# Kernel optimization log

Measured on AMD Instinct MI355X. Metric: run time of the kernel, lower is better.

Reference implementation:

```python
import jax, jax.numpy as jnp
import numpy as np

L, D_MODEL, D_INNER, D_STATE, D_CONV, DT_RANK, NUM_ORDERS = 16384, 192, 384, 16, 4, 12, 2
NUM_BLOCKS = 2 * NUM_ORDERS
EPS = 1e-5


def rmsnorm(x, w):
    return x * jax.lax.rsqrt(jnp.mean(x * x, axis=-1, keepdims=True) + EPS) * w


def layernorm(x, w, b):
    m = jnp.mean(x, axis=-1, keepdims=True)
    v = jnp.mean((x - m) ** 2, axis=-1, keepdims=True)
    return (x - m) * jax.lax.rsqrt(v + EPS) * w + b


def causal_dw_conv(x, w, b):
    # x: [L, d], w: [d, K] causal depthwise conv (small fixed K loop)
    K = w.shape[1]
    xp = jnp.pad(x, ((K - 1, 0), (0, 0)))
    y = b
    for k in range(K):
        y = y + xp[k:k + x.shape[0]] * w[:, k]
    return y


def selective_scan(u, dt, A, B, C, Dskip):
    # u, dt: [L, d]; A: [d, n]; B, C: [L, n]; Dskip: [d]
    def step(h, inp):
        u_t, dt_t, B_t, C_t = inp
        dA = jnp.exp(dt_t[:, None] * A)                    # [d, n]
        h = dA * h + (dt_t * u_t)[:, None] * B_t[None, :]  # [d, n]
        return h, h @ C_t                                  # y_t: [d]
    h0 = jnp.zeros(A.shape, u.dtype)
    _, ys = jax.lax.scan(step, h0, (u, dt, B, C))
    return ys + u * Dskip


def mamba_block(x, nw, Wi, cw, cb, Wx, Wdt, bdt, A_log, Dp, Wo):
    # pre-RMSNorm residual Mamba block (create_block semantics)
    res = x
    h = rmsnorm(x, nw)
    xz = h @ Wi                              # [L, 2*d_inner]
    xc, z = jnp.split(xz, 2, axis=-1)
    xc = jax.nn.silu(causal_dw_conv(xc, cw, cb))
    proj = xc @ Wx                           # [L, dt_rank + 2*d_state]
    dt_raw = proj[:, :DT_RANK]
    B = proj[:, DT_RANK:DT_RANK + D_STATE]
    C = proj[:, DT_RANK + D_STATE:]
    dt = jax.nn.softplus(dt_raw @ Wdt + bdt)
    y = selective_scan(xc, dt, -jnp.exp(A_log), B, C, Dp)
    y = y * jax.nn.silu(z)
    return res + y @ Wo


def setup_inputs() -> dict:
    key = jax.random.key(0)
    ks = jax.random.split(key, 10)
    s = 0.02
    x = jax.random.normal(ks[0], (L, D_MODEL), jnp.float32)
    orders = jnp.stack([
        jax.random.permutation(jax.random.fold_in(ks[1], o), L)
        for o in range(NUM_ORDERS)
    ]).astype(jnp.int32)                                     # [NUM_ORDERS, L]
    norm_w = jnp.ones((NUM_BLOCKS, D_MODEL), jnp.float32)
    in_proj_w = jax.random.normal(ks[2], (NUM_BLOCKS, D_MODEL, 2 * D_INNER), jnp.float32) * s
    conv_w = jax.random.normal(ks[3], (NUM_BLOCKS, D_INNER, D_CONV), jnp.float32) * s
    conv_b = jnp.zeros((NUM_BLOCKS, D_INNER), jnp.float32)
    x_proj_w = jax.random.normal(ks[4], (NUM_BLOCKS, D_INNER, DT_RANK + 2 * D_STATE), jnp.float32) * s
    dt_w = jax.random.normal(ks[5], (NUM_BLOCKS, DT_RANK, D_INNER), jnp.float32) * s
    dt_b = jnp.full((NUM_BLOCKS, D_INNER), np.log(np.expm1(0.01)), jnp.float32)  # softplus^-1(0.01)
    A_log = jnp.log(jnp.broadcast_to(jnp.arange(1, D_STATE + 1, dtype=jnp.float32),
                                     (NUM_BLOCKS, D_INNER, D_STATE)))
    D_p = jnp.ones((NUM_BLOCKS, D_INNER), jnp.float32)
    out_proj_w = jax.random.normal(ks[6], (NUM_BLOCKS, D_INNER, D_MODEL), jnp.float32) * s
    fwd_ln_w = jnp.ones((NUM_ORDERS, D_MODEL), jnp.float32)
    fwd_ln_b = jnp.zeros((NUM_ORDERS, D_MODEL), jnp.float32)
    bwd_ln_w = jnp.ones((NUM_ORDERS, D_MODEL), jnp.float32)
    bwd_ln_b = jnp.zeros((NUM_ORDERS, D_MODEL), jnp.float32)
    out_ln_w = jnp.ones((NUM_ORDERS, D_MODEL), jnp.float32)
    out_ln_b = jnp.zeros((NUM_ORDERS, D_MODEL), jnp.float32)
    return {"x": x, "orders": orders, "norm_w": norm_w, "in_proj_w": in_proj_w,
            "conv_w": conv_w, "conv_b": conv_b, "x_proj_w": x_proj_w,
            "dt_w": dt_w, "dt_b": dt_b, "A_log": A_log, "D_p": D_p,
            "out_proj_w": out_proj_w, "fwd_ln_w": fwd_ln_w, "fwd_ln_b": fwd_ln_b,
            "bwd_ln_w": bwd_ln_w, "bwd_ln_b": bwd_ln_b,
            "out_ln_w": out_ln_w, "out_ln_b": out_ln_b}


def reference(x, orders, norm_w, in_proj_w, conv_w, conv_b, x_proj_w, dt_w, dt_b,
              A_log, D_p, out_proj_w, fwd_ln_w, fwd_ln_b, bwd_ln_w, bwd_ln_b,
              out_ln_w, out_ln_b):
    out = x
    for o in range(NUM_ORDERS):          # small fixed loop over serialization orders
        idx = orders[o]
        xo = x[idx]                      # serialize voxel tokens in this order
        fb, bb = o, NUM_ORDERS + o       # forward / backward block indices
        f = mamba_block(xo, norm_w[fb], in_proj_w[fb], conv_w[fb], conv_b[fb],
                        x_proj_w[fb], dt_w[fb], dt_b[fb], A_log[fb], D_p[fb], out_proj_w[fb])
        b = mamba_block(xo[::-1], norm_w[bb], in_proj_w[bb], conv_w[bb], conv_b[bb],
                        x_proj_w[bb], dt_w[bb], dt_b[bb], A_log[bb], D_p[bb], out_proj_w[bb])[::-1]
        comb = layernorm(f, fwd_ln_w[o], fwd_ln_b[o]) + layernorm(b, bwd_ln_w[o], bwd_ln_b[o])
        comb = layernorm(comb, out_ln_w[o], out_ln_b[o])
        out = out + jnp.zeros_like(x).at[idx].set(comb)  # de-serialize (scatter back)
    return out
```

## Files before the change

kernel.cpp:

```cpp
#include <hip/hip_runtime.h>
#include <math.h>

#define LSEQ 16384
#define DM 192
#define DI 384
#define DSN 16
#define DCONV 4
#define DTRK 12
#define NPROJ 44
#define EPSV 1e-5f
#define TCH 32
#define NCH (LSEQ / TCH)
#define GDIM (DI * DSN)
#define RGRP 8
#define NGRP (NCH / RGRP)
#define CT 8

typedef __attribute__((ext_vector_type(8))) short bf16x8;
typedef __attribute__((ext_vector_type(4))) float f32x4;

__device__ __forceinline__ float siluf(float x) { return x / (1.f + __expf(-x)); }
__device__ __forceinline__ float softplus_f(float x) {
  float e = __expf(x);
  float l = __logf(1.f + e);
  return (x > 20.f) ? x : l;
}
__device__ __forceinline__ ushort f2b(float f) {
  uint u = __float_as_uint(f);
  u += 0x7fff + ((u >> 16) & 1);
  return (ushort)(u >> 16);
}
__device__ __forceinline__ float b2f(ushort h) { return __uint_as_float(((uint)h) << 16); }
__device__ __forceinline__ ushort f2h(float f) { _Float16 h = (_Float16)f; return *(ushort*)&h; }
__device__ __forceinline__ float h2f(ushort u) { _Float16 h = *(_Float16*)&u; return (float)h; }

__device__ __forceinline__ void pow16(float q, float (&a)[16]) {
  float q2 = q*q, q4 = q2*q2, q8 = q4*q4;
  a[0]=q;        a[1]=q2;       a[2]=q2*q;      a[3]=q4;
  a[4]=q4*q;     a[5]=q4*q2;    a[6]=q4*q2*q;   a[7]=q8;
  a[8]=q8*q;     a[9]=q8*q2;    a[10]=q8*q2*q;  a[11]=q8*q4;
  a[12]=q8*q4*q; a[13]=q8*q4*q2;a[14]=q8*q4*q2*q;a[15]=q8*q8;
}

#define PREP_A (4 * 768 * DM)
#define PREP_B (4 * 64 * DI)
#define PREP_C (4 * DM * DI)
__global__ void k_prep(const float* __restrict__ Wi, const float* __restrict__ nw,
                       const float* __restrict__ Wx, const float* __restrict__ Wo,
                       ushort* __restrict__ Wct, ushort* __restrict__ Wxt,
                       ushort* __restrict__ Wot) {
  int i = blockIdx.x * 256 + threadIdx.x;
  if (i < PREP_A) {
    int blk = i / (768 * DM), j = i % (768 * DM);
    int n = j / DM, k = j % DM;
    Wct[i] = f2b(nw[blk*DM + k] * Wi[(size_t)blk*DM*768 + (size_t)k*768 + n]);
  } else if (i < PREP_A + PREP_B) {
    int q = i - PREP_A;
    int blk = q / (64 * DI), j = q % (64 * DI);
    int n = j / DI, k = j % DI;
    Wxt[q] = (n < NPROJ) ? f2b(Wx[(size_t)blk*DI*NPROJ + (size_t)k*NPROJ + n]) : (ushort)0;
  } else if (i < PREP_A + PREP_B + PREP_C) {
    int q = i - PREP_A - PREP_B;
    int blk = q / (DM * DI), j = q % (DM * DI);
    int n = j / DI, k = j % DI;
    Wot[q] = f2b(Wo[(size_t)blk*DI*DM + (size_t)k*DM + n]);
  }
}

__global__ __launch_bounds__(64) void k_gather_rms(const float* __restrict__ x,
                                                   const int* __restrict__ orders,
                                                   ushort* __restrict__ xon) {
  int t = blockIdx.x;
  int o = blockIdx.y;
  int lane = threadIdx.x;
  int r = orders[(size_t)o*LSEQ + t];
  ushort* xo = xon + (size_t)o*LSEQ*DM;
  float v0 = x[(size_t)r*DM + lane];
  float v1 = x[(size_t)r*DM + 64 + lane];
  float v2 = x[(size_t)r*DM + 128 + lane];
  float ss = v0*v0 + v1*v1 + v2*v2;
  #pragma unroll
  for (int oo = 32; oo > 0; oo >>= 1) ss += __shfl_xor(ss, oo);
  float s = rsqrtf(ss * (1.f/DM) + EPSV);
  xo[(size_t)t*DM + lane]       = f2b(v0 * s);
  xo[(size_t)t*DM + 64 + lane]  = f2b(v1 * s);
  xo[(size_t)t*DM + 128 + lane] = f2b(v2 * s);
}

template<int MI, int AMODE, int OMODE>
__global__ __launch_bounds__(256) void k_mm(
    const ushort* __restrict__ A, const ushort* __restrict__ Yp,
    const ushort* __restrict__ Zp, const ushort* __restrict__ Bt,
    void* __restrict__ C0, void* __restrict__ C1,
    int N, int K, int lda, int ldz, int ldc,
    long sA, long sY, long sZ, long sB, long sC)
{
  __shared__ __align__(16) ushort As[32 * MI * 64];
  __shared__ __align__(16) ushort Bs[64 * 64];
  const int z = blockIdx.z;
  if (AMODE == 0) A += (size_t)z * sA;
  else { Yp += (size_t)z * sY; Zp += (size_t)z * sZ; }
  Bt += (size_t)z * sB;
  const int bm = blockIdx.x * (32 * MI), bn = blockIdx.y * 64;
  const int tid = threadIdx.x;
  const int l = tid & 63, w = tid >> 6;
  const int wm = w & 1, wn = w >> 1;
  f32x4 acc[MI][2] = {};

  for (int k0 = 0; k0 < K; k0 += 64) {
    #pragma unroll
    for (int p = 0; p < MI; p++) {
      int c = tid + p * 256;
      int row = c >> 3, ko = (c & 7) * 8;
      int sw = (row * 128 + (c & 7) * 16) ^ ((row & 7) << 4);
      if (AMODE == 0) {
        uint4 v = *(const uint4*)(A + (size_t)(bm + row) * lda + k0 + ko);
        *(uint4*)((char*)As + sw) = v;
      } else {
        const ushort* yrow = Yp + (size_t)(bm + row) * lda + k0 + ko;
        const ushort* zrow = Zp + (size_t)(bm + row) * ldz + k0 + ko;
        ushort tmp[8];
        #pragma unroll
        for (int j = 0; j < 8; j++) {
          float zz = b2f(zrow[j]);
          tmp[j] = f2b(b2f(yrow[j]) * (zz / (1.f + __expf(-zz))));
        }
        *(uint4*)((char*)As + sw) = *(const uint4*)tmp;
      }
    }
    #pragma unroll
    for (int p = 0; p < 2; p++) {
      int c = tid + p * 256;
      int row = c >> 3, ko = (c & 7) * 8;
      int sw = (row * 128 + (c & 7) * 16) ^ ((row & 7) << 4);
      uint4 v = *(const uint4*)(Bt + (size_t)(bn + row) * K + k0 + ko);
      *(uint4*)((char*)Bs + sw) = v;
    }
    __syncthreads();
    #pragma unroll
    for (int ks = 0; ks < 2; ks++) {
      bf16x8 af[MI], bfv[2];
      #pragma unroll
      for (int mi = 0; mi < MI; mi++) {
        int r = 16 * MI * wm + 16 * mi + (l & 15);
        int ad = (r * 128 + 32 * ks + 16 * (l >> 4)) ^ ((r & 7) << 4);
        af[mi] = *(const bf16x8*)((const char*)As + ad);
      }
      #pragma unroll
      for (int ni = 0; ni < 2; ni++) {
        int r = 32 * wn + 16 * ni + (l & 15);
        int ad = (r * 128 + 32 * ks + 16 * (l >> 4)) ^ ((r & 7) << 4);
        bfv[ni] = *(const bf16x8*)((const char*)Bs + ad);
      }
      #pragma unroll
      for (int mi = 0; mi < MI; mi++)
        #pragma unroll
        for (int ni = 0; ni < 2; ni++)
          acc[mi][ni] = __builtin_amdgcn_mfma_f32_16x16x32_bf16(
              af[mi], bfv[ni], acc[mi][ni], 0, 0, 0);
    }
    __syncthreads();
  }

  #pragma unroll
  for (int mi = 0; mi < MI; mi++) {
    #pragma unroll
    for (int ni = 0; ni < 2; ni++) {
      int c0 = bn + 32 * wn + 16 * ni + (l & 15);
      if (OMODE != 2 && c0 >= N) continue;
      int r0 = bm + 16 * MI * wm + 16 * mi + 4 * (l >> 4);
      #pragma unroll
      for (int j = 0; j < 4; j++) {
        if (OMODE == 0) {
          ((float*)C0 + (size_t)z*sC)[(size_t)(r0 + j) * ldc + c0] = acc[mi][ni][j];
        } else if (OMODE == 1) {
          ((ushort*)C0 + (size_t)z*sC)[(size_t)(r0 + j) * ldc + c0] = f2b(acc[mi][ni][j]);
        } else {
          if (c0 < 384)
            ((ushort*)C0 + (size_t)z*sC)[(size_t)(r0 + j) * 384 + c0] = f2b(acc[mi][ni][j]);
          else
            ((ushort*)C1 + (size_t)z*sC)[(size_t)(r0 + j) * 384 + (c0 - 384)] = f2b(acc[mi][ni][j]);
        }
      }
    }
  }
}

__global__ __launch_bounds__(256) void k_conv(const ushort* __restrict__ XC,
                                              const float* __restrict__ cw,
                                              const float* __restrict__ cb,
                                              ushort* __restrict__ U, int o) {
  int z = blockIdx.y;
  int blk = o + 2*z;
  int sgn = 1 - 2*z;
  int i = blockIdx.x * 256 + threadIdx.x;
  if (i >= (LSEQ/CT) * (DI/8)) return;
  int tb = i / (DI/8), d0 = (i % (DI/8)) * 8;
  const ushort* X = XC + (size_t)z*LSEQ*DI;
  ushort* Uz = U + (size_t)z*LSEQ*DI;

  float wv[4][8];
  #pragma unroll
  for (int j = 0; j < 8; j++) {
    float4 t4 = *(const float4*)(cw + (size_t)blk*DI*DCONV + (d0+j)*DCONV);
    wv[0][j]=t4.x; wv[1][j]=t4.y; wv[2][j]=t4.z; wv[3][j]=t4.w;
  }
  float cbv[8];
  *(float4*)&cbv[0] = *(const float4*)(cb + blk*DI + d0);
  *(float4*)&cbv[4] = *(const float4*)(cb + blk*DI + d0 + 4);

  int tau0 = tb * CT;
  float win[3][8];
  #pragma unroll
  for (int q = 0; q < 3; q++) {
    int tau = tau0 - 3 + q;
    if (tau >= 0) {
      int r = (sgn > 0) ? tau : (LSEQ-1-tau);
      uint4 xv = *(const uint4*)(X + (size_t)r*DI + d0);
      const ushort* xs = (const ushort*)&xv;
      #pragma unroll
      for (int j = 0; j < 8; j++) win[q][j] = b2f(xs[j]);
    } else {
      #pragma unroll
      for (int j = 0; j < 8; j++) win[q][j] = 0.f;
    }
  }
  #pragma unroll
  for (int tt = 0; tt < CT; tt++) {
    int tau = tau0 + tt;
    int r = (sgn > 0) ? tau : (LSEQ-1-tau);
    float cur[8];
    uint4 xv = *(const uint4*)(X + (size_t)r*DI + d0);
    const ushort* xs = (const ushort*)&xv;
    #pragma unroll
    for (int j = 0; j < 8; j++) cur[j] = b2f(xs[j]);
    ushort outv[8];
    #pragma unroll
    for (int j = 0; j < 8; j++) {
      float a = cbv[j];
      a = fmaf(wv[0][j], win[0][j], a);
      a = fmaf(wv[1][j], win[1][j], a);
      a = fmaf(wv[2][j], win[2][j], a);
      a = fmaf(wv[3][j], cur[j],    a);
      outv[j] = f2b(siluf(a));
    }
    *(uint4*)(Uz + (size_t)r*DI + d0) = *(const uint4*)outv;
    #pragma unroll
    for (int j = 0; j < 8; j++) {
      win[0][j] = win[1][j]; win[1][j] = win[2][j]; win[2][j] = cur[j];
    }
  }
}

__global__ __launch_bounds__(128) void k_scan1(const ushort* __restrict__ UC,
                                               const float* __restrict__ PROJ,
                                               const float* __restrict__ Alog,
                                               const float* __restrict__ Wdt,
                                               const float* __restrict__ bdt,
                                               const float* __restrict__ Dp,
                                               float* __restrict__ Dc,
                                               ushort* __restrict__ Sc,
                                               ushort* __restrict__ CDT,
                                               ushort* __restrict__ Y, int o) {
  __shared__ float Ps[TCH][NPROJ];
  int z = blockIdx.z;
  int blk = o + 2*z;
  int sgn = 1 - 2*z;
  const ushort* Uz = UC + (size_t)z*LSEQ*DI;
  const float* Pz = PROJ + (size_t)z*LSEQ*NPROJ;
  ushort* CDTz = CDT + (size_t)z*LSEQ*DI;
  ushort* Yz = Y + (size_t)z*LSEQ*DI;
  int c = blockIdx.y;
  int dd = blockIdx.x * 128;
  int tid = threadIdx.x;
  int d = dd + tid;
  for (int j = tid; j < TCH * 11; j += 128) {
    int row = j / 11, q4 = j % 11;
    int s = c*TCH + row;
    int rg = (sgn > 0) ? s : (LSEQ-1-s);
    *(float4*)&Ps[row][q4*4] = *(const float4*)(Pz + (size_t)rg*NPROJ + q4*4);
  }
  __syncthreads();

  float wdt[DTRK];
  #pragma unroll
  for (int k = 0; k < DTRK; k++) wdt[k] = Wdt[(size_t)blk*DTRK*DI + k*DI + d];
  float bdtv = bdt[blk*DI + d];
  const float* Ablk = Alog + (size_t)blk*DI*DSN + (size_t)d*DSN;
  bool fast = true;
  #pragma unroll
  for (int n = 0; n < DSN; n++) {
    float An = -__expf(Ablk[n]);
    fast = fast && (fabsf(An + (float)(n+1)) <= 1e-3f * (n+1));
  }
  float dskip = Dp[blk*DI + d];
  float S[DSN] = {};
  float dtsum = 0.f;
  for (int t = 0; t < TCH; t++) {
    int s = c*TCH + t;
    int row = (sgn > 0) ? s : (LSEQ-1-s);
    float u = b2f(Uz[(size_t)row*DI + d]);
    const float* pr = &Ps[t][0];
    float dtp[12], Bv[DSN], Cv[DSN];
    *(float4*)&dtp[0] = *(const float4*)(pr + 0);
    *(float4*)&dtp[4] = *(const float4*)(pr + 4);
    *(float4*)&dtp[8] = *(const float4*)(pr + 8);
    *(float4*)&Bv[0]  = *(const float4*)(pr + 12);
    *(float4*)&Bv[4]  = *(const float4*)(pr + 16);
    *(float4*)&Bv[8]  = *(const float4*)(pr + 20);
    *(float4*)&Bv[12] = *(const float4*)(pr + 24);
    *(float4*)&Cv[0]  = *(const float4*)(pr + 28);
    *(float4*)&Cv[4]  = *(const float4*)(pr + 32);
    *(float4*)&Cv[8]  = *(const float4*)(pr + 36);
    *(float4*)&Cv[12] = *(const float4*)(pr + 40);
    float xdt = bdtv;
    #pragma unroll
    for (int k = 0; k < DTRK; k++) xdt = fmaf(dtp[k], wdt[k], xdt);
    float dtv = softplus_f(xdt);
    float du = dtv * u;
    dtsum += dtv;
    float a[DSN];
    if (fast) { pow16(__expf(-dtv), a); }
    else {
      #pragma unroll
      for (int n = 0; n < DSN; n++) a[n] = __expf(dtv * -__expf(Ablk[n]));
    }
    float y = u * dskip;
    #pragma unroll
    for (int n = 0; n < DSN; n++) {
      S[n] = a[n] * S[n] + du * Bv[n];
      y += S[n] * Cv[n];
    }
    Yz[(size_t)row * DI + d] = f2b(y);
    CDTz[(size_t)row * DI + d] = f2h(dtsum);
  }
  Dc[(size_t)z*NCH*DI + (size_t)c*DI + d] = dtsum;
  ushort st[16];
  #pragma unroll
  for (int n = 0; n < DSN; n++) st[n] = f2b(S[n]);
  ushort* sp = Sc + (size_t)z*NCH*GDIM + (size_t)c*GDIM + (size_t)d*DSN;
  *(uint4*)sp       = *(const uint4*)&st[0];
  *(uint4*)(sp + 8) = *(const uint4*)&st[8];
}

__global__ __launch_bounds__(256) void k_scan2a(const float* __restrict__ Dc,
                                                const ushort* __restrict__ Sc,
                                                const float* __restrict__ Alog,
                                                float* __restrict__ PL,
                                                float* __restrict__ SL, int o) {
  int g = blockIdx.x * 256 + threadIdx.x;
  int l = blockIdx.y;
  int z = blockIdx.z;
  int blk = o + 2*z;
  int d = g >> 4;
  float A = -__expf(Alog[(size_t)blk*GDIM + g]);
  const float* Dz = Dc + (size_t)z*NCH*DI;
  const ushort* Sz = Sc + (size_t)z*NCH*GDIM;
  float Da = 0.f, Sa = 0.f;
  #pragma unroll
  for (int j = 0; j < RGRP; j++) {
    int c = l*RGRP + j;
    float D = Dz[(size_t)c*DI + d];
    float p = __expf(A * D);
    Sa = fmaf(p, Sa, b2f(Sz[(size_t)c*GDIM + g]));
    Da += D;
  }
  PL[(size_t)z*NGRP*GDIM + (size_t)l * GDIM + g] = __expf(A * Da);
  SL[(size_t)z*NGRP*GDIM + (size_t)l * GDIM + g] = Sa;
}

__global__ __launch_bounds__(256) void k_scan2b(const float* __restrict__ PL,
                                                const float* __restrict__ SL,
                                                float* __restrict__ HL) {
  int g = blockIdx.x * 256 + threadIdx.x;
  int z = blockIdx.y;
  const float* Pz = PL + (size_t)z*NGRP*GDIM;
  const float* Sz = SL + (size_t)z*NGRP*GDIM;
  float* Hz = HL + (size_t)z*NGRP*GDIM;
  float p[NGRP], s[NGRP];
  #pragma unroll
  for (int l = 0; l < NGRP; l++) {
    p[l] = Pz[(size_t)l * GDIM + g];
    s[l] = Sz[(size_t)l * GDIM + g];
  }
  float H = 0.f;
  #pragma unroll
  for (int l = 0; l < NGRP; l++) {
    Hz[(size_t)l * GDIM + g] = H;
    H = fmaf(p[l], H, s[l]);
  }
}

__global__ __launch_bounds__(256) void k_scan2c(const float* __restrict__ Dc,
                                                const ushort* __restrict__ Sc,
                                                const float* __restrict__ HL,
                                                const float* __restrict__ Alog,
                                                ushort* __restrict__ Hc, int o) {
  int g = blockIdx.x * 256 + threadIdx.x;
  int l = blockIdx.y;
  int z = blockIdx.z;
  int blk = o + 2*z;
  int d = g >> 4;
  float A = -__expf(Alog[(size_t)blk*GDIM + g]);
  const float* Dz = Dc + (size_t)z*NCH*DI;
  const ushort* Sz = Sc + (size_t)z*NCH*GDIM;
  float h = HL[(size_t)z*NGRP*GDIM + (size_t)l * GDIM + g];
  ushort* Hz = Hc + (size_t)z*NCH*GDIM;
  #pragma unroll
  for (int j = 0; j < RGRP; j++) {
    int c = l*RGRP + j;
    size_t off = (size_t)c * GDIM + g;
    Hz[off] = f2b(h);
    float p = __expf(A * Dz[(size_t)c*DI + d]);
    h = fmaf(p, h, b2f(Sz[off]));
  }
}

__global__ __launch_bounds__(128) void k_fix(const ushort* __restrict__ Hc,
                                             const ushort* __restrict__ CDT,
                                             const float* __restrict__ PROJ,
                                             const float* __restrict__ Alog,
                                             ushort* __restrict__ Y, int o) {
  __shared__ float Cs[TCH][DSN];
  int z = blockIdx.z;
  int c = blockIdx.y;
  int blk = o + 2*z;
  int sgn = 1 - 2*z;
  int dd = blockIdx.x * 128;
  int tid = threadIdx.x;
  int d = dd + tid;
  const float* Pz = PROJ + (size_t)z*LSEQ*NPROJ;
  const ushort* CDTz = CDT + (size_t)z*LSEQ*DI;
  ushort* Yz = Y + (size_t)z*LSEQ*DI;

  {
    int row = tid >> 2, q4 = tid & 3;
    int s = c*TCH + row;
    int rg = (sgn > 0) ? s : (LSEQ-1-s);
    *(float4*)&Cs[row][q4*4] = *(const float4*)(Pz + (size_t)rg*NPROJ + 28 + q4*4);
  }

  const float* Ablk = Alog + (size_t)blk*DI*DSN + (size_t)d*DSN;
  bool fast = true;
  #pragma unroll
  for (int n = 0; n < DSN; n++) {
    float An = -__expf(Ablk[n]);
    fast = fast && (fabsf(An + (float)(n+1)) <= 1e-3f * (n+1));
  }
  float h[DSN];
  {
    const ushort* hp = Hc + (size_t)z*NCH*GDIM + (size_t)c*GDIM + (size_t)d*DSN;
    uint4 h0 = *(const uint4*)hp;
    uint4 h1 = *(const uint4*)(hp + 8);
    const ushort* hs0 = (const ushort*)&h0;
    const ushort* hs1 = (const ushort*)&h1;
    #pragma unroll
    for (int n = 0; n < 8; n++) { h[n] = b2f(hs0[n]); h[8+n] = b2f(hs1[n]); }
  }
  __syncthreads();

  for (int t = 0; t < TCH; t++) {
    int s = c*TCH + t;
    int row = (sgn > 0) ? s : (LSEQ-1-s);
    float cd = h2f(CDTz[(size_t)row*DI + d]);
    float p[DSN];
    if (fast) { pow16(__expf(-cd), p); }
    else {
      #pragma unroll
      for (int n = 0; n < DSN; n++) p[n] = __expf(cd * -__expf(Ablk[n]));
    }
    float Cv[DSN];
    *(float4*)&Cv[0]  = *(const float4*)&Cs[t][0];
    *(float4*)&Cv[4]  = *(const float4*)&Cs[t][4];
    *(float4*)&Cv[8]  = *(const float4*)&Cs[t][8];
    *(float4*)&Cv[12] = *(const float4*)&Cs[t][12];
    float corr = 0.f;
    #pragma unroll
    for (int n = 0; n < DSN; n++)
      corr = fmaf(p[n] * h[n], Cv[n], corr);
    size_t yi = (size_t)row*DI + d;
    Yz[yi] = f2b(b2f(Yz[yi]) + corr);
  }
}

__device__ __forceinline__ void ln_row(float (&v)[3], const float* __restrict__ w,
                                       const float* __restrict__ b, int lane) {
  float s = v[0] + v[1] + v[2];
  #pragma unroll
  for (int o = 32; o > 0; o >>= 1) s += __shfl_xor(s, o);
  float m = s * (1.f / DM);
  float q = 0.f;
  #pragma unroll
  for (int i = 0; i < 3; i++) { float d = v[i] - m; q += d*d; }
  #pragma unroll
  for (int o = 32; o > 0; o >>= 1) q += __shfl_xor(q, o);
  float inv = rsqrtf(q * (1.f / DM) + EPSV);
  #pragma unroll
  for (int i = 0; i < 3; i++) v[i] = (v[i] - m) * inv * w[lane + 64*i] + b[lane + 64*i];
}

template<int FIRST>
__global__ __launch_bounds__(64) void k_final(const float* __restrict__ x,
                                              const int* __restrict__ idx,
                                              const ushort* __restrict__ G4f,
                                              const ushort* __restrict__ G4b,
                                              const float* __restrict__ lnfw,
                                              const float* __restrict__ lnfb,
                                              const float* __restrict__ lnbw,
                                              const float* __restrict__ lnbb,
                                              const float* __restrict__ lnow,
                                              const float* __restrict__ lnob,
                                              float* __restrict__ out) {
  int t = blockIdx.x, lane = threadIdx.x;
  int r = idx[t];
  float f[3], g[3], cb[3];
  #pragma unroll
  for (int i = 0; i < 3; i++) {
    int j = lane + 64*i;
    float xo = x[(size_t)r*DM + j];
    f[i] = xo + b2f(G4f[(size_t)t*DM + j]);
    g[i] = xo + b2f(G4b[(size_t)t*DM + j]);
  }
  ln_row(f, lnfw, lnfb, lane);
  ln_row(g, lnbw, lnbb, lane);
  #pragma unroll
  for (int i = 0; i < 3; i++) cb[i] = f[i] + g[i];
  ln_row(cb, lnow, lnob, lane);
  #pragma unroll
  for (int i = 0; i < 3; i++) {
    int j = lane + 64*i;
    if (FIRST)
      out[(size_t)r*DM + j] = x[(size_t)r*DM + j] + cb[i];
    else
      out[(size_t)r*DM + j] += cb[i];
  }
}

extern "C" void kernel_launch(void* const* d_in, const int* in_sizes, int n_in,
                              void* d_out, int out_size, void* d_ws, size_t ws_size,
                              hipStream_t stream) {
  const float* x      = (const float*)d_in[0];
  const int*   orders = (const int*)  d_in[1];
  const float* nw     = (const float*)d_in[2];
  const float* Wi     = (const float*)d_in[3];
  const float* cw     = (const float*)d_in[4];
  const float* cbi    = (const float*)d_in[5];
  const float* Wx     = (const float*)d_in[6];
  const float* Wdt    = (const float*)d_in[7];
  const float* bdt    = (const float*)d_in[8];
  const float* Alog   = (const float*)d_in[9];
  const float* Dp     = (const float*)d_in[10];
  const float* Wo     = (const float*)d_in[11];
  const float* flw    = (const float*)d_in[12];
  const float* flb    = (const float*)d_in[13];
  const float* blw    = (const float*)d_in[14];
  const float* blb    = (const float*)d_in[15];
  const float* olw    = (const float*)d_in[16];
  const float* olb    = (const float*)d_in[17];
  float* outp = (float*)d_out;

  char* w = (char*)d_ws;
  size_t off = 0;
  auto take = [&](size_t bytes) -> void* {
    char* p = w + off;
    off += (bytes + 255) & ~(size_t)255;
    return (void*)p;
  };
  ushort* Wct  = (ushort*)take((size_t)4 * 768 * DM * 2);
  ushort* Wxt  = (ushort*)take((size_t)4 * 64 * DI * 2);
  ushort* Wot  = (ushort*)take((size_t)4 * DM * DI * 2);
  ushort* xon  = (ushort*)take((size_t)2 * LSEQ * DM * 2);
  ushort* xc   = (ushort*)take((size_t)2 * LSEQ * DI * 2);
  ushort* zc   = (ushort*)take((size_t)2 * LSEQ * DI * 2);
  ushort* uc   = (ushort*)take((size_t)2 * LSEQ * DI * 2);
  ushort* ybuf = (ushort*)take((size_t)2 * LSEQ * DI * 2);
  ushort* cdt  = (ushort*)take((size_t)2 * LSEQ * DI * 2);
  float*  proj = (float*) take((size_t)2 * LSEQ * NPROJ * 4);
  ushort* g4   = (ushort*)take((size_t)2 * LSEQ * DM * 2);
  float*  Dc   = (float*) take((size_t)2 * NCH * DI * 4);
  ushort* Sc   = (ushort*)take((size_t)2 * NCH * GDIM * 2);
  ushort* Hc   = (ushort*)take((size_t)2 * NCH * GDIM * 2);
  float*  PL   = (float*) take((size_t)2 * NGRP * GDIM * 4);
  float*  SL   = (float*) take((size_t)2 * NGRP * GDIM * 4);
  float*  HL   = (float*) take((size_t)2 * NGRP * GDIM * 4);
  (void)ws_size; (void)n_in; (void)in_sizes; (void)out_size;

  k_prep<<<(PREP_A + PREP_B + PREP_C + 255)/256, 256, 0, stream>>>(
      Wi, nw, Wx, Wo, Wct, Wxt, Wot);
  k_gather_rms<<<dim3(LSEQ, 2), 64, 0, stream>>>(x, orders, xon);

  for (int o = 0; o < 2; o++) {
    const int* idx = orders + (size_t)o * LSEQ;

    k_mm<4,0,2><<<dim3(LSEQ/128, 768/64, 2), 256, 0, stream>>>(
        xon + (size_t)o*LSEQ*DM, nullptr, nullptr, Wct + (size_t)o*768*DM,
        xc, zc, 768, DM, DM, 0, 384,
        0L, 0L, 0L, (long)2*768*DM, (long)LSEQ*DI);
    k_conv<<<dim3(((LSEQ/CT)*(DI/8) + 255)/256, 2), 256, 0, stream>>>(
        xc, cw, cbi, uc, o);
    k_mm<2,0,0><<<dim3(LSEQ/64, 1, 2), 256, 0, stream>>>(
        uc, nullptr, nullptr, Wxt + (size_t)o*64*DI,
        proj, nullptr, NPROJ, DI, DI, 0, NPROJ,
        (long)LSEQ*DI, 0L, 0L, (long)2*64*DI, (long)LSEQ*NPROJ);
    k_scan1<<<dim3(DI/128, NCH, 2), 128, 0, stream>>>(
        uc, proj, Alog, Wdt, bdt, Dp, Dc, Sc, cdt, ybuf, o);
    k_scan2a<<<dim3(GDIM/256, NGRP, 2), 256, 0, stream>>>(Dc, Sc, Alog, PL, SL, o);
    k_scan2b<<<dim3(GDIM/256, 2), 256, 0, stream>>>(PL, SL, HL);
    k_scan2c<<<dim3(GDIM/256, NGRP, 2), 256, 0, stream>>>(Dc, Sc, HL, Alog, Hc, o);
    k_fix<<<dim3(DI/128, NCH, 2), 128, 0, stream>>>(
        Hc, cdt, proj, Alog, ybuf, o);
    k_mm<2,1,1><<<dim3(LSEQ/64, DM/64, 2), 256, 0, stream>>>(
        nullptr, ybuf, zc, Wot + (size_t)o*DM*DI,
        g4, nullptr, DM, DI, DI, DI, DM,
        0L, (long)LSEQ*DI, (long)LSEQ*DI, (long)2*DM*DI, (long)LSEQ*DM);

    if (o == 0)
      k_final<1><<<LSEQ, 64, 0, stream>>>(x, idx, g4, g4 + (size_t)LSEQ*DM,
          flw, flb, blw, blb, olw, olb, outp);
    else
      k_final<0><<<LSEQ, 64, 0, stream>>>(x, idx, g4, g4 + (size_t)LSEQ*DM,
          flw + (size_t)DM, flb + (size_t)DM,
          blw + (size_t)DM, blb + (size_t)DM,
          olw + (size_t)DM, olb + (size_t)DM, outp);
  }
}
```

Baseline: 362.9 us.

## Batch all four Mamba blocks into single launches and recompute dt in fix pass

Replaces the per-order loop with one launch per stage covering all four blocks (two orders times forward/backward), so each grid has twice as many blocks and half as many kernel launches. Block index z now selects weights directly, and direction comes from z>>1. It also drops the fp16 cumulative-dt buffer written by scan1 and read by fix. Instead, fix recomputes softplus(dt_raw·Wdt+b) from the projection rows held in shared memory and keeps a running sum. ybuf and Hc alias the xc and uc buffers to limit workspace growth, at the cost of extra arithmetic in the fix kernel and a larger working set.

New measurement: 334.1 us, median of 2. -7.9%, faster.

```diff
diff --git a/kernel.cpp b/kernel.cpp
--- a/kernel.cpp
+++ b/kernel.cpp
@@ -16,6 +16,7 @@
 #define NGRP (NCH / RGRP)
 #define CT 8
 
+
 typedef __attribute__((ext_vector_type(8))) short bf16x8;
 typedef __attribute__((ext_vector_type(4))) float f32x4;
 
@@ -31,8 +32,6 @@
   return (ushort)(u >> 16);
 }
 __device__ __forceinline__ float b2f(ushort h) { return __uint_as_float(((uint)h) << 16); }
-__device__ __forceinline__ ushort f2h(float f) { _Float16 h = (_Float16)f; return *(ushort*)&h; }
-__device__ __forceinline__ float h2f(ushort u) { _Float16 h = *(_Float16*)&u; return (float)h; }
 
 __device__ __forceinline__ void pow16(float q, float (&a)[16]) {
   float q2 = q*q, q4 = q2*q2, q8 = q4*q4;
@@ -92,13 +91,13 @@
     const ushort* __restrict__ A, const ushort* __restrict__ Yp,
     const ushort* __restrict__ Zp, const ushort* __restrict__ Bt,
     void* __restrict__ C0, void* __restrict__ C1,
-    int N, int K, int lda, int ldz, int ldc,
+    int N, int K, int lda, int ldz, int ldc, int aMask,
     long sA, long sY, long sZ, long sB, long sC)
 {
   __shared__ __align__(16) ushort As[32 * MI * 64];
   __shared__ __align__(16) ushort Bs[64 * 64];
   const int z = blockIdx.z;
-  if (AMODE == 0) A += (size_t)z * sA;
+  if (AMODE == 0) A += (size_t)(z & aMask) * sA;
   else { Yp += (size_t)z * sY; Zp += (size_t)z * sZ; }
   Bt += (size_t)z * sB;
   const int bm = blockIdx.x * (32 * MI), bn = blockIdx.y * 64;
@@ -189,10 +188,10 @@
 __global__ __launch_bounds__(256) void k_conv(const ushort* __restrict__ XC,
                                               const float* __restrict__ cw,
                                               const float* __restrict__ cb,
-                                              ushort* __restrict__ U, int o) {
+                                              ushort* __restrict__ U) {
   int z = blockIdx.y;
-  int blk = o + 2*z;
-  int sgn = 1 - 2*z;
+  int blk = z;
+  int sgn = 1 - 2*(z >> 1);
   int i = blockIdx.x * 256 + threadIdx.x;
   if (i >= (LSEQ/CT) * (DI/8)) return;
   int tb = i / (DI/8), d0 = (i % (DI/8)) * 8;
@@ -260,15 +259,13 @@
                                                const float* __restrict__ Dp,
                                                float* __restrict__ Dc,
                                                ushort* __restrict__ Sc,
-                                               ushort* __restrict__ CDT,
-                                               ushort* __restrict__ Y, int o) {
+                                               ushort* __restrict__ Y) {
   __shared__ float Ps[TCH][NPROJ];
   int z = blockIdx.z;
-  int blk = o + 2*z;
-  int sgn = 1 - 2*z;
+  int blk = z;
+  int sgn = 1 - 2*(z >> 1);
   const ushort* Uz = UC + (size_t)z*LSEQ*DI;
   const float* Pz = PROJ + (size_t)z*LSEQ*NPROJ;
-  ushort* CDTz = CDT + (size_t)z*LSEQ*DI;
   ushort* Yz = Y + (size_t)z*LSEQ*DI;
   int c = blockIdx.y;
   int dd = blockIdx.x * 128;
@@ -286,7 +283,7 @@
   #pragma unroll
   for (int k = 0; k < DTRK; k++) wdt[k] = Wdt[(size_t)blk*DTRK*DI + k*DI + d];
   float bdtv = bdt[blk*DI + d];
-  const float* Ablk = Alog + (size_t)blk*DI*DSN + (size_t)d*DSN;
+  const float* Ablk = Alog + (size_t)blk*GDIM + (size_t)d*DSN;
   bool fast = true;
   #pragma unroll
   for (int n = 0; n < DSN; n++) {
@@ -332,7 +329,6 @@
       y += S[n] * Cv[n];
     }
     Yz[(size_t)row * DI + d] = f2b(y);
-    CDTz[(size_t)row * DI + d] = f2h(dtsum);
   }
   Dc[(size_t)z*NCH*DI + (size_t)c*DI + d] = dtsum;
   ushort st[16];
@@ -347,11 +343,11 @@
                                                 const ushort* __restrict__ Sc,
                                                 const float* __restrict__ Alog,
                                                 float* __restrict__ PL,
-                                                float* __restrict__ SL, int o) {
+                                                float* __restrict__ SL) {
   int g = blockIdx.x * 256 + threadIdx.x;
   int l = blockIdx.y;
   int z = blockIdx.z;
-  int blk = o + 2*z;
+  int blk = z;
   int d = g >> 4;
   float A = -__expf(Alog[(size_t)blk*GDIM + g]);
   const float* Dz = Dc + (size_t)z*NCH*DI;
@@ -395,11 +391,11 @@
                                                 const ushort* __restrict__ Sc,
                                                 const float* __restrict__ HL,
                                                 const float* __restrict__ Alog,
-                                                ushort* __restrict__ Hc, int o) {
+                                                ushort* __restrict__ Hc) {
   int g = blockIdx.x * 256 + threadIdx.x;
   int l = blockIdx.y;
   int z = blockIdx.z;
-  int blk = o + 2*z;
+  int blk = z;
   int d = g >> 4;
   float A = -__expf(Alog[(size_t)blk*GDIM + g]);
   const float* Dz = Dc + (size_t)z*NCH*DI;
@@ -417,22 +413,29 @@
 }
 
 __global__ __launch_bounds__(128) void k_fix(const ushort* __restrict__ Hc,
-                                             const ushort* __restrict__ CDT,
                                              const float* __restrict__ PROJ,
                                              const float* __restrict__ Alog,
-                                             ushort* __restrict__ Y, int o) {
+                                             const float* __restrict__ Wdt,
+                                             const float* __restrict__ bdt,
+                                             ushort* __restrict__ Y) {
+  __shared__ float Dts[TCH][DTRK];
   __shared__ float Cs[TCH][DSN];
   int z = blockIdx.z;
   int c = blockIdx.y;
-  int blk = o + 2*z;
-  int sgn = 1 - 2*z;
+  int blk = z;
+  int sgn = 1 - 2*(z >> 1);
   int dd = blockIdx.x * 128;
   int tid = threadIdx.x;
   int d = dd + tid;
   const float* Pz = PROJ + (size_t)z*LSEQ*NPROJ;
-  const ushort* CDTz = CDT + (size_t)z*LSEQ*DI;
   ushort* Yz = Y + (size_t)z*LSEQ*DI;
 
+  for (int j = tid; j < TCH * 3; j += 128) {
+    int row = j / 3, q4 = j % 3;
+    int s = c*TCH + row;
+    int rg = (sgn > 0) ? s : (LSEQ-1-s);
+    *(float4*)&Dts[row][q4*4] = *(const float4*)(Pz + (size_t)rg*NPROJ + q4*4);
+  }
   {
     int row = tid >> 2, q4 = tid & 3;
     int s = c*TCH + row;
@@ -440,7 +443,11 @@
     *(float4*)&Cs[row][q4*4] = *(const float4*)(Pz + (size_t)rg*NPROJ + 28 + q4*4);
   }
 
-  const float* Ablk = Alog + (size_t)blk*DI*DSN + (size_t)d*DSN;
+  float wdt[DTRK];
+  #pragma unroll
+  for (int k = 0; k < DTRK; k++) wdt[k] = Wdt[(size_t)blk*DTRK*DI + k*DI + d];
+  float bdtv = bdt[blk*DI + d];
+  const float* Ablk = Alog + (size_t)blk*GDIM + (size_t)d*DSN;
   bool fast = true;
   #pragma unroll
   for (int n = 0; n < DSN; n++) {
@@ -459,21 +466,28 @@
   }
   __syncthreads();
 
+  float cd = 0.f;
   for (int t = 0; t < TCH; t++) {
     int s = c*TCH + t;
     int row = (sgn > 0) ? s : (LSEQ-1-s);
-    float cd = h2f(CDTz[(size_t)row*DI + d]);
-    float p[DSN];
-    if (fast) { pow16(__expf(-cd), p); }
-    else {
-      #pragma unroll
-      for (int n = 0; n < DSN; n++) p[n] = __expf(cd * -__expf(Ablk[n]));
-    }
-    float Cv[DSN];
+    float dtp[12], Cv[DSN];
+    *(float4*)&dtp[0] = *(const float4*)&Dts[t][0];
+    *(float4*)&dtp[4] = *(const float4*)&Dts[t][4];
+    *(float4*)&dtp[8] = *(const float4*)&Dts[t][8];
     *(float4*)&Cv[0]  = *(const float4*)&Cs[t][0];
     *(float4*)&Cv[4]  = *(const float4*)&Cs[t][4];
     *(float4*)&Cv[8]  = *(const float4*)&Cs[t][8];
     *(float4*)&Cv[12] = *(const float4*)&Cs[t][12];
+    float xdt = bdtv;
+    #pragma unroll
+    for (int k = 0; k < DTRK; k++) xdt = fmaf(dtp[k], wdt[k], xdt);
+    cd += softplus_f(xdt);
+    float p[DSN];
+    if (fast) { pow16(__expf(-cd), p); }
+    else {
+      #pragma unroll
+      for (int n = 0; n < DSN; n++) p[n] = __expf(cd * -__expf(Ablk[n]));
+    }
     float corr = 0.f;
     #pragma unroll
     for (int n = 0; n < DSN; n++)
@@ -570,57 +584,46 @@
   ushort* Wxt  = (ushort*)take((size_t)4 * 64 * DI * 2);
   ushort* Wot  = (ushort*)take((size_t)4 * DM * DI * 2);
   ushort* xon  = (ushort*)take((size_t)2 * LSEQ * DM * 2);
-  ushort* xc   = (ushort*)take((size_t)2 * LSEQ * DI * 2);
-  ushort* zc   = (ushort*)take((size_t)2 * LSEQ * DI * 2);
-  ushort* uc   = (ushort*)take((size_t)2 * LSEQ * DI * 2);
-  ushort* ybuf = (ushort*)take((size_t)2 * LSEQ * DI * 2);
-  ushort* cdt  = (ushort*)take((size_t)2 * LSEQ * DI * 2);
-  float*  proj = (float*) take((size_t)2 * LSEQ * NPROJ * 4);
-  ushort* g4   = (ushort*)take((size_t)2 * LSEQ * DM * 2);
-  float*  Dc   = (float*) take((size_t)2 * NCH * DI * 4);
-  ushort* Sc   = (ushort*)take((size_t)2 * NCH * GDIM * 2);
-  ushort* Hc   = (ushort*)take((size_t)2 * NCH * GDIM * 2);
-  float*  PL   = (float*) take((size_t)2 * NGRP * GDIM * 4);
-  float*  SL   = (float*) take((size_t)2 * NGRP * GDIM * 4);
-  float*  HL   = (float*) take((size_t)2 * NGRP * GDIM * 4);
+  ushort* xc   = (ushort*)take((size_t)4 * LSEQ * DI * 2);
+  ushort* zc   = (ushort*)take((size_t)4 * LSEQ * DI * 2);
+  ushort* uc   = (ushort*)take((size_t)4 * LSEQ * DI * 2);
+  float*  proj = (float*) take((size_t)4 * LSEQ * NPROJ * 4);
+  ushort* g4   = (ushort*)take((size_t)4 * LSEQ * DM * 2);
+  float*  Dc   = (float*) take((size_t)4 * NCH * DI * 4);
+  ushort* Sc   = (ushort*)take((size_t)4 * NCH * GDIM * 2);
+  float*  PL   = (float*) take((size_t)4 * NGRP * GDIM * 4);
+  float*  SL   = (float*) take((size_t)4 * NGRP * GDIM * 4);
+  float*  HL   = (float*) take((size_t)4 * NGRP * GDIM * 4);
+  ushort* ybuf = xc;
+  ushort* Hc   = uc;
   (void)ws_size; (void)n_in; (void)in_sizes; (void)out_size;
 
   k_prep<<<(PREP_A + PREP_B + PREP_C + 255)/256, 256, 0, stream>>>(
       Wi, nw, Wx, Wo, Wct, Wxt, Wot);
   k_gather_rms<<<dim3(LSEQ, 2), 64, 0, stream>>>(x, orders, xon);
 
-  for (int o = 0; o < 2; o++) {
-    const int* idx = orders + (size_t)o * LSEQ;
-
-    k_mm<4,0,2><<<dim3(LSEQ/128, 768/64, 2), 256, 0, stream>>>(
-        xon + (size_t)o*LSEQ*DM, nullptr, nullptr, Wct + (size_t)o*768*DM,
-        xc, zc, 768, DM, DM, 0, 384,
-        0L, 0L, 0L, (long)2*768*DM, (long)LSEQ*DI);
-    k_conv<<<dim3(((LSEQ/CT)*(DI/8) + 255)/256, 2), 256, 0, stream>>>(
-        xc, cw, cbi, uc, o);
-    k_mm<2,0,0><<<dim3(LSEQ/64, 1, 2), 256, 0, stream>>>(
-        uc, nullptr, nullptr, Wxt + (size_t)o*64*DI,
-        proj, nullptr, NPROJ, DI, DI, 0, NPROJ,
-        (long)LSEQ*DI, 0L, 0L, (long)2*64*DI, (long)LSEQ*NPROJ);
-    k_scan1<<<dim3(DI/128, NCH, 2), 128, 0, stream>>>(
-        uc, proj, Alog, Wdt, bdt, Dp, Dc, Sc, cdt, ybuf, o);
-    k_scan2a<<<dim3(GDIM/256, NGRP, 2), 256, 0, stream>>>(Dc, Sc, Alog, PL, SL, o);
-    k_scan2b<<<dim3(GDIM/256, 2), 256, 0, stream>>>(PL, SL, HL);
-    k_scan2c<<<dim3(GDIM/256, NGRP, 2), 256, 0, stream>>>(Dc, Sc, HL, Alog, Hc, o);
-    k_fix<<<dim3(DI/128, NCH, 2), 128, 0, stream>>>(
-        Hc, cdt, proj, Alog, ybuf, o);
-    k_mm<2,1,1><<<dim3(LSEQ/64, DM/64, 2), 256, 0, stream>>>(
-        nullptr, ybuf, zc, Wot + (size_t)o*DM*DI,
-        g4, nullptr, DM, DI, DI, DI, DM,
-        0L, (long)LSEQ*DI, (long)LSEQ*DI, (long)2*DM*DI, (long)LSEQ*DM);
-
-    if (o == 0)
-      k_final<1><<<LSEQ, 64, 0, stream>>>(x, idx, g4, g4 + (size_t)LSEQ*DM,
-          flw, flb, blw, blb, olw, olb, outp);
-    else
-      k_final<0><<<LSEQ, 64, 0, stream>>>(x, idx, g4, g4 + (size_t)LSEQ*DM,
-          flw + (size_t)DM, flb + (size_t)DM,
-          blw + (size_t)DM, blb + (size_t)DM,
-          olw + (size_t)DM, olb + (size_t)DM, outp);
-  }
-}
+  k_mm<4,0,2><<<dim3(LSEQ/128, 768/64, 4), 256, 0, stream>>>(
+      xon, nullptr, nullptr, Wct, xc, zc, 768, DM, DM, 0, 384, 1,
+      (long)LSEQ*DM, 0L, 0L, (long)768*DM, (long)LSEQ*DI);
+  k_conv<<<dim3(((LSEQ/CT)*(DI/8) + 255)/256, 4), 256, 0, stream>>>(
+      xc, cw, cbi, uc);
+  k_mm<2,0,0><<<dim3(LSEQ/64, 1, 4), 256, 0, stream>>>(
+      uc, nullptr, nullptr, Wxt, proj, nullptr, NPROJ, DI, DI, 0, NPROJ, 3,
+      (long)LSEQ*DI, 0L, 0L, (long)64*DI, (long)LSEQ*NPROJ);
+  k_scan1<<<dim3(DI/128, NCH, 4), 128, 0, stream>>>(
+      uc, proj, Alog, Wdt, bdt, Dp, Dc, Sc, ybuf);
+  k_scan2a<<<dim3(GDIM/256, NGRP, 4), 256, 0, stream>>>(Dc, Sc, Alog, PL, SL);
+  k_scan2b<<<dim3(GDIM/256, 4), 256, 0, stream>>>(PL, SL, HL);
+  k_scan2c<<<dim3(GDIM/256, NGRP, 4), 256, 0, stream>>>(Dc, Sc, HL, Alog, Hc);
+  k_fix<<<dim3(DI/128, NCH, 4), 128, 0, stream>>>(
+      Hc, proj, Alog, Wdt, bdt, ybuf);
+  k_mm<2,1,1><<<dim3(LSEQ/64, DM/64, 4), 256, 0, stream>>>(
+      nullptr, ybuf, zc, Wot, g4, nullptr, DM, DI, DI, DI, DM, 3,
+      0L, (long)LSEQ*DI, (long)LSEQ*DI, (long)DM*DI, (long)LSEQ*DM);
+
+  k_final<1><<<LSEQ, 64, 0, stream>>>(x, orders, g4, g4 + (size_t)2*LSEQ*DM,
+      flw, flb, blw, blb, olw, olb, outp);
+  k_final<0><<<LSEQ, 64, 0, stream>>>(x, orders + LSEQ,
+      g4 + (size_t)1*LSEQ*DM, g4 + (size_t)3*LSEQ*DM,
+      flw + DM, flb + DM, blw + DM, blb + DM, olw + DM, olb + DM, outp);
+}
```
